# Kernel tuning notes

Measured on AMD Instinct MI355X. Metric: run time of the kernel, lower is better.

The kernel has to match this reference:

```python
import math
import jax, jax.numpy as jnp
import numpy as np

D_MODEL = 1024
N_HEADS = 16
D_FF = 4096
B = 4
T = 1024  # tgt len
S = 1024  # src len
EPS = 1e-6


def _linear_params(key, d_in, d_out):
    kw, kb = jax.random.split(key)
    w = jax.random.normal(kw, (d_out, d_in), dtype=jnp.float32) * 0.02
    b = jax.random.normal(kb, (d_out,), dtype=jnp.float32) * 0.02
    return w, b


def setup_inputs() -> dict:
    key = jax.random.key(0)
    ks = jax.random.split(key, 16)
    x = jax.random.normal(ks[0], (B, T, D_MODEL), dtype=jnp.float32)
    memory = jax.random.normal(ks[1], (B, S, D_MODEL), dtype=jnp.float32)
    # causal [B, T, T] mask (dim==3 branch) and padding [B, S] mask (dim==2 branch)
    tgt_mask = jnp.broadcast_to(jnp.tril(jnp.ones((T, T), dtype=jnp.int32)), (B, T, T))
    src_mask = jnp.ones((B, S), dtype=jnp.int32)
    inp = {"x": x, "memory": memory, "tgt_mask": tgt_mask, "src_mask": src_mask}
    names = ["sa_wq", "sa_wk", "sa_wv", "sa_wo", "ca_wq", "ca_wk", "ca_wv", "ca_wo"]
    for i, n in enumerate(names):
        w, b = _linear_params(ks[2 + i], D_MODEL, D_MODEL)
        inp[n] = w
        inp[n.replace("w", "b")] = b
    inp["ff_w1"], inp["ff_b1"] = _linear_params(ks[10], D_MODEL, D_FF)
    inp["ff_w2"], inp["ff_b2"] = _linear_params(ks[11], D_FF, D_MODEL)
    for i, n in enumerate(["ln1", "ln2", "ln3"]):
        inp[n + "_w"] = jnp.ones((D_MODEL,), dtype=jnp.float32)
        inp[n + "_b"] = jnp.zeros((D_MODEL,), dtype=jnp.float32)
    return inp


def layernorm(x, w, b):
    # torch-faithful: unbiased std (N-1), eps added to std (not variance)
    mean = jnp.mean(x, axis=-1, keepdims=True)
    d = x - mean
    std = jnp.sqrt(jnp.sum(d * d, axis=-1, keepdims=True) / (x.shape[-1] - 1))
    return w * d / (std + EPS) + b


def mha(q_in, kv_in, mask, wq, bq, wk, bk, wv, bv, wo, bo):
    Bb, Tq, D = q_in.shape
    Tk = kv_in.shape[1]
    dk = D // N_HEADS
    if mask.ndim == 2:
        mask4 = mask[:, None, None, :]
    else:
        mask4 = mask[:, None, :, :]
    q = (q_in @ wq.T + bq).reshape(Bb, Tq, N_HEADS, dk).transpose(0, 2, 1, 3)
    k = (kv_in @ wk.T + bk).reshape(Bb, Tk, N_HEADS, dk).transpose(0, 2, 1, 3)
    v = (kv_in @ wv.T + bv).reshape(Bb, Tk, N_HEADS, dk).transpose(0, 2, 1, 3)
    scores = jnp.einsum("bhqd,bhkd->bhqk", q, k) / math.sqrt(dk)
    scores = jnp.where(mask4 == 0, jnp.float32(-1e9), scores)
    attn = jax.nn.softmax(scores, axis=-1)
    out = jnp.einsum("bhqk,bhkd->bhqd", attn, v)
    out = out.transpose(0, 2, 1, 3).reshape(Bb, Tq, D)
    return out @ wo.T + bo


def reference(x, memory, tgt_mask, src_mask,
              sa_wq, sa_bq, sa_wk, sa_bk, sa_wv, sa_bv, sa_wo, sa_bo,
              ca_wq, ca_bq, ca_wk, ca_bk, ca_wv, ca_bv, ca_wo, ca_bo,
              ff_w1, ff_b1, ff_w2, ff_b2,
              ln1_w, ln1_b, ln2_w, ln2_b, ln3_w, ln3_b):
    # pre-norm decoder block (norm_first=True), dropout=0 (eval)
    h = layernorm(x, ln1_w, ln1_b)
    x = x + mha(h, h, tgt_mask, sa_wq, sa_bq, sa_wk, sa_bk, sa_wv, sa_bv, sa_wo, sa_bo)
    h = layernorm(x, ln2_w, ln2_b)
    x = x + mha(h, memory, src_mask, ca_wq, ca_bq, ca_wk, ca_bk, ca_wv, ca_bv, ca_wo, ca_bo)
    h = layernorm(x, ln3_w, ln3_b)
    x = x + (jax.nn.relu(h @ ff_w1.T + ff_b1) @ ff_w2.T + ff_b2)
    return x
```

## Files before the change

### kernel.cpp

```cpp
#include <hip/hip_runtime.h>
#include <hip/hip_bf16.h>

typedef unsigned short u16;
typedef __attribute__((ext_vector_type(4))) float f32x4;
typedef __attribute__((ext_vector_type(8))) short s16x8;
typedef __attribute__((ext_vector_type(4))) short s16x4;
typedef __attribute__((ext_vector_type(8))) __bf16 bf16x8;

#define NTOK 4096
#define DMODEL 1024
#define DFF 4096
#define NH 16
#define TSEQ 1024


__device__ __forceinline__ u16 f2b_hw(float f) {
  union { __bf16 h; u16 u; } cv;
  cv.h = (__bf16)f;
  return cv.u;
}

__device__ __forceinline__ f32x4 mfma16(s16x8 a, s16x8 b, f32x4 c) {
  return __builtin_amdgcn_mfma_f32_16x16x32_bf16((bf16x8)a, (bf16x8)b, c, 0, 0, 0);
}

__device__ __forceinline__ void gload16(const u16* g, u16* l) {
  __builtin_amdgcn_global_load_lds(
      (const __attribute__((address_space(1))) unsigned int*)g,
      (__attribute__((address_space(3))) unsigned int*)l, 16, 0, 0);
}

__device__ __forceinline__ s16x8 ld8s(const u16* t, int row, int eoff) {
  int rx = row & 7;
  const u16* p1 = t + row * 64 + ((((eoff >> 3) ^ rx) << 3) | (eoff & 7));
  const u16* p2 = t + row * 64 + (((((eoff + 16) >> 3) ^ rx) << 3) | (eoff & 7));
  s16x4 lo = *(const s16x4*)p1;
  s16x4 hi = *(const s16x4*)p2;
  s16x8 r;
  r[0] = lo[0]; r[1] = lo[1]; r[2] = lo[2]; r[3] = lo[3];
  r[4] = hi[0]; r[5] = hi[1]; r[6] = hi[2]; r[7] = hi[3];
  return r;
}

__device__ __forceinline__ s16x8 ld16s(const u16* t, int row, int ch) {
  return *(const s16x8*)(t + row * 64 + ((ch ^ (row & 7)) << 3));
}


struct F2B {
  const float* s[11];
  u16* d[11];
};

__global__ __launch_bounds__(256) void f2b_all(F2B a) {
  int bid = blockIdx.x;
  int seg, boff;
  if (bid < 8192) { seg = bid >> 10; boff = bid & 1023; }
  else { int j = bid - 8192; seg = 8 + (j >> 12); boff = j & 4095; }
  size_t i = ((size_t)boff * 256 + threadIdx.x) * 4;
  float4 v = *(const float4*)(a.s[seg] + i);
  ushort4 o = make_ushort4(f2b_hw(v.x), f2b_hw(v.y), f2b_hw(v.z), f2b_hw(v.w));
  *(ushort4*)(a.d[seg] + i) = o;
}


__global__ __launch_bounds__(256) void ln_kernel(const float* __restrict__ x,
                                                 const float* __restrict__ w,
                                                 const float* __restrict__ b,
                                                 u16* __restrict__ out) {
  int row = blockIdx.x;
  int t = threadIdx.x;
  const float* xr = x + (size_t)row * DMODEL;
  float4 v = *(const float4*)(xr + t * 4);
  float s = v.x + v.y + v.z + v.w;
#pragma unroll
  for (int off = 1; off < 64; off <<= 1) s += __shfl_xor(s, off);
  __shared__ float red[8];
  int wid = t >> 6, lane = t & 63;
  if (lane == 0) red[wid] = s;
  __syncthreads();
  float mean = (red[0] + red[1] + red[2] + red[3]) * (1.0f / 1024.0f);
  float dx = v.x - mean, dy = v.y - mean, dz = v.z - mean, dw = v.w - mean;
  float ss = dx * dx + dy * dy + dz * dz + dw * dw;
#pragma unroll
  for (int off = 1; off < 64; off <<= 1) ss += __shfl_xor(ss, off);
  if (lane == 0) red[4 + wid] = ss;
  __syncthreads();
  float sst = red[4] + red[5] + red[6] + red[7];
  float inv = 1.0f / (sqrtf(sst / 1023.0f) + 1e-6f);
  float4 wv = *(const float4*)(w + t * 4);
  float4 bv = *(const float4*)(b + t * 4);
  ushort4 o = make_ushort4(f2b_hw(wv.x * dx * inv + bv.x), f2b_hw(wv.y * dy * inv + bv.y),
                           f2b_hw(wv.z * dz * inv + bv.z), f2b_hw(wv.w * dw * inv + bv.w));
  *(ushort4*)(out + (size_t)row * DMODEL + t * 4) = o;
}


template <int MODE, bool RELU, bool SPLITK = false, int QBUF = -1, int VBUF = -1>
__global__ __launch_bounds__(512) void gemm_bt(const u16* __restrict__ A,
                                               const u16* __restrict__ W,
                                               const float* __restrict__ b0,
                                               const float* __restrict__ b1,
                                               const float* __restrict__ b2,
                                               const float* resid, void* outp,
                                               int M, int N, int K, int ld,
                                               int gx) {
  __shared__ u16 As[2][128 * 64];
  __shared__ u16 Bs[2][128 * 64];
  const int nwg = gridDim.x;
  const int qch = nwg >> 3;
  const int bid = blockIdx.x;
  int wg = (bid & 7) * qch + (bid >> 3);
  int half = 0;
  if (SPLITK) { half = wg & 1; wg >>= 1; }
  const int bx = wg % gx, by = wg / gx;
  const int m0 = by * 128, n0 = bx * 128;
  if (SPLITK) { A += (size_t)half * K; W += (size_t)half * K; }
  const int tid = threadIdx.x;
  const int wid = tid >> 6, lane = tid & 63;
  const int wr = wid >> 2, wc = wid & 3;
  const int lhi = lane >> 4, llo = lane & 15;
  f32x4 acc[4][2] = {};
  const int sr = tid >> 3, sc = tid & 7;
  const int srcoff = (sc ^ (sr & 7)) << 3;

  auto stage = [&](int kk, int buf) {
    const u16* Ap = A + (size_t)(m0 + sr) * ld + kk + srcoff;
    gload16(Ap, &As[buf][tid * 8]);
    gload16(Ap + (size_t)64 * ld, &As[buf][4096 + tid * 8]);
    const u16* Wp = W + (size_t)(n0 + sr) * ld + kk + srcoff;
    gload16(Wp, &Bs[buf][tid * 8]);
    gload16(Wp + (size_t)64 * ld, &Bs[buf][4096 + tid * 8]);
  };

  stage(0, 0);
  __syncthreads();

  for (int k0 = 0; k0 < K; k0 += 64) {
    int cur = (k0 >> 6) & 1;
    if (k0 + 64 < K) stage(k0 + 64, cur ^ 1);
#pragma unroll
    for (int ks8 = 0; ks8 < 8; ks8 += 4) {
      s16x8 af[4], bfr[2];
#pragma unroll
      for (int f = 0; f < 4; f++) af[f] = ld16s(&As[cur][0], wr * 64 + f * 16 + llo, ks8 + lhi);
#pragma unroll
      for (int g = 0; g < 2; g++) bfr[g] = ld16s(&Bs[cur][0], wc * 32 + g * 16 + llo, ks8 + lhi);
#pragma unroll
      for (int f = 0; f < 4; f++)
#pragma unroll
        for (int g = 0; g < 2; g++) acc[f][g] = mfma16(af[f], bfr[g], acc[f][g]);
    }
    __syncthreads();
  }

#pragma unroll
  for (int fm = 0; fm < 4; fm++) {
#pragma unroll
    for (int fn = 0; fn < 2; fn++) {
      int c = n0 + wc * 32 + fn * 16 + llo;
      const int r0 = m0 + wr * 64 + fm * 16 + lhi * 4;
      if (MODE == 2) {
        int buf = c >> 10, cc = c & 1023;
        int hh = cc >> 6, d = cc & 63;
        int bb = r0 >> 10, t0 = r0 & 1023;
        const float* bias = (buf == 0) ? b0 : ((buf == 1) ? b1 : b2);
        float bv = bias[cc];
        float v4[4];
#pragma unroll
        for (int i = 0; i < 4; i++) {
          float v = acc[fm][fn][i] + bv;
          if (buf == QBUF) v *= 0.125f;
          v4[i] = v;
        }
        if (buf == VBUF) {
          ushort4 st = make_ushort4(f2b_hw(v4[0]), f2b_hw(v4[1]), f2b_hw(v4[2]), f2b_hw(v4[3]));
          *(ushort4*)(&((u16*)outp)[(size_t)buf * 4194304 +
                                    (((size_t)(bb * NH + hh)) * 64 + d) * TSEQ + t0]) = st;
        } else {
#pragma unroll
          for (int i = 0; i < 4; i++)
            ((u16*)outp)[(size_t)buf * 4194304 +
                         (((size_t)(bb * NH + hh)) * TSEQ + t0 + i) * 64 + d] = f2b_hw(v4[i]);
        }
      } else {
        float bv = b0 ? b0[c] : 0.0f;
#pragma unroll
        for (int i = 0; i < 4; i++) {
          int r = r0 + i;
          float v = acc[fm][fn][i] + bv;
          if (resid) v += resid[(size_t)r * N + c];
          if (RELU) v = fmaxf(v, 0.0f);
          if (MODE == 0) {
            ((float*)outp)[(size_t)half * M * N + (size_t)r * N + c] = v;
          } else {
            ((u16*)outp)[(size_t)r * N + c] = f2b_hw(v);
          }
        }
      }
    }
  }
}


__global__ __launch_bounds__(256) void ff2_reduce(const float* __restrict__ p,
                                                  const float* __restrict__ bias,
                                                  float* __restrict__ out) {
  int row = blockIdx.x, t = threadIdx.x;
  size_t i = (size_t)row * 1024 + t * 4;
  const float* p1 = p + (size_t)4194304;
  float4 a = *(const float4*)(p + i);
  float4 b = *(const float4*)(p1 + i);
  float4 r = *(const float4*)(out + i);
  float4 bv = *(const float4*)(bias + t * 4);
  float4 o = make_float4(a.x + b.x + r.x + bv.x, a.y + b.y + r.y + bv.y,
                         a.z + b.z + r.z + bv.z, a.w + b.w + r.w + bv.w);
  *(float4*)(out + i) = o;
}


template <bool CAUSAL>
__global__ __launch_bounds__(256) void attn_kernel(const u16* __restrict__ Qg,
                                                   const u16* __restrict__ Kg,
                                                   const u16* __restrict__ Vt,
                                                   u16* __restrict__ Og) {
  const int bid = blockIdx.x;
  const int wg = (bid & 7) * 64 + (bid >> 3);
  const int bh = wg >> 3, qblk = wg & 7;
  const int b = bh >> 4, h = bh & 15;
  const int q0 = qblk * 128;
  const int tid = threadIdx.x, wid = tid >> 6, lane = tid & 63;
  const int lhi = lane >> 4, llo = lane & 15;
  __shared__ u16 Ks[2][4096];
  __shared__ u16 Vs[2][4096];

  const int qr = q0 + wid * 16 + llo;
  const u16* qp0 = Qg + ((size_t)bh * TSEQ + qr) * 64;
  s16x8 qf[2][2];
  qf[0][0] = *(const s16x8*)(qp0 + 8 * lhi);
  qf[0][1] = *(const s16x8*)(qp0 + 8 * (4 + lhi));
  qf[1][0] = *(const s16x8*)(qp0 + 4096 + 8 * lhi);
  qf[1][1] = *(const s16x8*)(qp0 + 4096 + 8 * (4 + lhi));

  f32x4 oacc[2][4] = {};
  float mrun[2] = {-1.0e30f, -1.0e30f}, lrun[2] = {0.0f, 0.0f};
  const size_t kvb = (size_t)bh * (TSEQ * 64);
  const int nt = CAUSAL ? ((q0 + 128) >> 6) : (TSEQ >> 6);

  const int srow = tid >> 3;
  const int ssw = ((tid & 7) ^ (srow & 7)) << 3;

  auto stageK = [&](int s0, int buf) {
    const u16* kb = Kg + kvb + (size_t)s0 * 64;
    gload16(kb + (size_t)srow * 64 + ssw, &Ks[buf][tid * 8]);
    gload16(kb + (size_t)(32 + srow) * 64 + ssw, &Ks[buf][2048 + tid * 8]);
  };
  auto stageV = [&](int s0, int buf) {
    const u16* vb2 = Vt + kvb + s0;
    gload16(vb2 + (size_t)srow * TSEQ + ssw, &Vs[buf][tid * 8]);
    gload16(vb2 + (size_t)(32 + srow) * TSEQ + ssw, &Vs[buf][2048 + tid * 8]);
  };

  stageK(0, 0);
  stageV(0, 0);
  __syncthreads();

  for (int t = 0; t < nt; ++t) {
    int cur = t & 1;
    if (t + 1 < nt) {
      stageK((t + 1) * 64, cur ^ 1);
      stageV((t + 1) * 64, cur ^ 1);
    }
    int s0 = t * 64;
    const bool act0 = !CAUSAL || (s0 < q0 + 64);

    s16x8 kf[4][2];
#pragma unroll
    for (int g = 0; g < 4; g++) {
      kf[g][0] = ld16s(&Ks[cur][0], g * 16 + llo, lhi);
      kf[g][1] = ld16s(&Ks[cur][0], g * 16 + llo, 4 + lhi);
    }

    s16x8 pf[2][2];
#pragma unroll
    for (int s = 0; s < 2; s++) {
      if (s == 0 && !act0) continue;
      f32x4 sacc[4] = {};
#pragma unroll
      for (int g = 0; g < 4; g++) {
        sacc[g] = mfma16(kf[g][0], qf[s][0], sacc[g]);
        sacc[g] = mfma16(kf[g][1], qf[s][1], sacc[g]);
      }
      const int qrow = qr + s * 64;
      const bool diag = CAUSAL && (s0 == q0 + s * 64);
      float sv[16];
      float pmax = -1.0e30f;
#pragma unroll
      for (int g = 0; g < 4; g++)
#pragma unroll
        for (int i = 0; i < 4; i++) {
          float sc = sacc[g][i];
          if (diag) {
            int kv = s0 + g * 16 + lhi * 4 + i;
            if (kv > qrow) sc = -1.0e9f;
          }
          sv[g * 4 + i] = sc;
          pmax = fmaxf(pmax, sc);
        }
      pmax = fmaxf(pmax, __shfl_xor(pmax, 16));
      pmax = fmaxf(pmax, __shfl_xor(pmax, 32));
      if (!__all(pmax - mrun[s] <= 8.0f)) {
        float mnew = fmaxf(mrun[s], pmax);
        float alpha = __expf(mrun[s] - mnew);
        lrun[s] *= alpha;
#pragma unroll
        for (int g = 0; g < 4; g++) {
          oacc[s][g][0] *= alpha; oacc[s][g][1] *= alpha;
          oacc[s][g][2] *= alpha; oacc[s][g][3] *= alpha;
        }
        mrun[s] = mnew;
      }
      float ls = 0.0f;
#pragma unroll
      for (int j = 0; j < 16; j++) {
        float p = __expf(sv[j] - mrun[s]);
        ls += p;
        pf[s][j >> 3][((j >> 2) & 1) * 4 + (j & 3)] = (short)f2b_hw(p);
      }
      ls += __shfl_xor(ls, 16);
      ls += __shfl_xor(ls, 32);
      lrun[s] += ls;
    }

#pragma unroll
    for (int dg = 0; dg < 4; dg++) {
      int row = dg * 16 + llo;
      s16x8 vf0 = ld8s(&Vs[cur][0], row, lhi * 4);
      s16x8 vf1 = ld8s(&Vs[cur][0], row, 32 + lhi * 4);
      if (act0) {
        oacc[0][dg] = mfma16(vf0, pf[0][0], oacc[0][dg]);
        oacc[0][dg] = mfma16(vf1, pf[0][1], oacc[0][dg]);
      }
      oacc[1][dg] = mfma16(vf0, pf[1][0], oacc[1][dg]);
      oacc[1][dg] = mfma16(vf1, pf[1][1], oacc[1][dg]);
    }

    __syncthreads();
  }

#pragma unroll
  for (int s = 0; s < 2; s++) {
    float inv = 1.0f / lrun[s];
    u16* orow = Og + (size_t)(b * TSEQ + qr + s * 64) * DMODEL + h * 64;
#pragma unroll
    for (int dg = 0; dg < 4; dg++) {
      ushort4 st = make_ushort4(f2b_hw(oacc[s][dg][0] * inv), f2b_hw(oacc[s][dg][1] * inv),
                                f2b_hw(oacc[s][dg][2] * inv), f2b_hw(oacc[s][dg][3] * inv));
      *(ushort4*)(orow + dg * 16 + lhi * 4) = st;
    }
  }
}


extern "C" void kernel_launch(void* const* d_in, const int* in_sizes, int n_in,
                              void* d_out, int out_size, void* d_ws, size_t ws_size,
                              hipStream_t stream) {
  const float* x      = (const float*)d_in[0];
  const float* memory = (const float*)d_in[1];
  const float* sa_wq = (const float*)d_in[4];  const float* sa_bq = (const float*)d_in[5];
  const float* sa_wk = (const float*)d_in[6];  const float* sa_bk = (const float*)d_in[7];
  const float* sa_wv = (const float*)d_in[8];  const float* sa_bv = (const float*)d_in[9];
  const float* sa_wo = (const float*)d_in[10]; const float* sa_bo = (const float*)d_in[11];
  const float* ca_wq = (const float*)d_in[12]; const float* ca_bq = (const float*)d_in[13];
  const float* ca_wk = (const float*)d_in[14]; const float* ca_bk = (const float*)d_in[15];
  const float* ca_wv = (const float*)d_in[16]; const float* ca_bv = (const float*)d_in[17];
  const float* ca_wo = (const float*)d_in[18]; const float* ca_bo = (const float*)d_in[19];
  const float* ff_w1 = (const float*)d_in[20]; const float* ff_b1 = (const float*)d_in[21];
  const float* ff_w2 = (const float*)d_in[22]; const float* ff_b2 = (const float*)d_in[23];
  const float* ln1_w = (const float*)d_in[24]; const float* ln1_b = (const float*)d_in[25];
  const float* ln2_w = (const float*)d_in[26]; const float* ln2_b = (const float*)d_in[27];
  const float* ln3_w = (const float*)d_in[28]; const float* ln3_b = (const float*)d_in[29];
  float* out = (float*)d_out;

  char* ws = (char*)d_ws;
  const size_t MB = 1u << 20;
  u16* h_bf   = (u16*)(ws + 0 * MB);
  u16* mem_bf = (u16*)(ws + 8 * MB);
  u16* qb     = (u16*)(ws + 16 * MB);
  u16* kb     = (u16*)(ws + 24 * MB);
  u16* vb     = (u16*)(ws + 32 * MB);
  u16* attnb  = (u16*)(ws + 40 * MB);
  u16* ffmid  = (u16*)(ws + 48 * MB);
  float* pk   = (float*)(ws + 16 * MB);
  u16* w_sq   = (u16*)(ws + 80 * MB);
  u16* w_sk   = (u16*)(ws + 82 * MB);
  u16* w_sv   = (u16*)(ws + 84 * MB);
  u16* w_so   = (u16*)(ws + 86 * MB);
  u16* w_cq   = (u16*)(ws + 88 * MB);
  u16* w_ck   = (u16*)(ws + 90 * MB);
  u16* w_cv   = (u16*)(ws + 92 * MB);
  u16* w_co   = (u16*)(ws + 94 * MB);
  u16* w_f1   = (u16*)(ws + 96 * MB);
  u16* w_f2   = (u16*)(ws + 104 * MB);

  F2B fa;
  fa.s[0] = sa_wq; fa.d[0] = w_sq;
  fa.s[1] = sa_wk; fa.d[1] = w_sk;
  fa.s[2] = sa_wv; fa.d[2] = w_sv;
  fa.s[3] = sa_wo; fa.d[3] = w_so;
  fa.s[4] = ca_wq; fa.d[4] = w_cq;
  fa.s[5] = ca_wk; fa.d[5] = w_ck;
  fa.s[6] = ca_wv; fa.d[6] = w_cv;
  fa.s[7] = ca_wo; fa.d[7] = w_co;
  fa.s[8] = ff_w1; fa.d[8] = w_f1;
  fa.s[9] = ff_w2; fa.d[9] = w_f2;
  fa.s[10] = memory; fa.d[10] = mem_bf;
  f2b_all<<<20480, 256, 0, stream>>>(fa);

  ln_kernel<<<4096, 256, 0, stream>>>(x, ln1_w, ln1_b, h_bf);
  gemm_bt<2, false, false, 0, 2><<<768, 512, 0, stream>>>(
      h_bf, w_sq, sa_bq, sa_bk, sa_bv, nullptr, qb, NTOK, 3072, DMODEL, DMODEL, 24);
  attn_kernel<true><<<512, 256, 0, stream>>>(qb, kb, vb, attnb);
  gemm_bt<0, false><<<256, 512, 0, stream>>>(attnb, w_so, sa_bo, nullptr, nullptr,
                                             x, out, NTOK, DMODEL, DMODEL, DMODEL, 8);

  ln_kernel<<<4096, 256, 0, stream>>>(out, ln2_w, ln2_b, h_bf);
  gemm_bt<2, false, false, 0, -1><<<256, 512, 0, stream>>>(
      h_bf, w_cq, ca_bq, nullptr, nullptr, nullptr, qb, NTOK, DMODEL, DMODEL, DMODEL, 8);
  gemm_bt<2, false, false, -1, 1><<<512, 512, 0, stream>>>(
      mem_bf, w_ck, ca_bk, ca_bv, nullptr, nullptr, kb, NTOK, 2048, DMODEL, DMODEL, 16);
  attn_kernel<false><<<512, 256, 0, stream>>>(qb, kb, vb, attnb);
  gemm_bt<0, false><<<256, 512, 0, stream>>>(attnb, w_co, ca_bo, nullptr, nullptr,
                                             out, out, NTOK, DMODEL, DMODEL, DMODEL, 8);

  ln_kernel<<<4096, 256, 0, stream>>>(out, ln3_w, ln3_b, h_bf);
  gemm_bt<1, true><<<1024, 512, 0, stream>>>(h_bf, w_f1, ff_b1, nullptr, nullptr,
                                             nullptr, ffmid, NTOK, DFF, DMODEL, DMODEL, 32);
  gemm_bt<0, false, true><<<512, 512, 0, stream>>>(ffmid, w_f2, nullptr, nullptr, nullptr,
                                                   nullptr, pk, NTOK, DMODEL, 2048, DFF, 8);
  ff2_reduce<<<4096, 256, 0, stream>>>(pk, ff_b2, out);

  (void)in_sizes; (void)n_in; (void)out_size; (void)ws_size;
}
```

Baseline: 332.8 us.

## Add 128x256-tile triple-buffered GEMM kernel for wide projection GEMMs

```diff
diff --git a/kernel.cpp b/kernel.cpp
--- a/kernel.cpp
+++ b/kernel.cpp
@@ -12,6 +12,8 @@
 #define DFF 4096
 #define NH 16
 #define TSEQ 1024
+
+#define SBAR() do { asm volatile("" ::: "memory"); __builtin_amdgcn_s_barrier(); asm volatile("" ::: "memory"); } while (0)
 
 
 __device__ __forceinline__ u16 f2b_hw(float f) {
@@ -93,6 +95,127 @@
   ushort4 o = make_ushort4(f2b_hw(wv.x * dx * inv + bv.x), f2b_hw(wv.y * dy * inv + bv.y),
                            f2b_hw(wv.z * dz * inv + bv.z), f2b_hw(wv.w * dw * inv + bv.w));
   *(ushort4*)(out + (size_t)row * DMODEL + t * 4) = o;
+}
+
+
+template <int MODE, bool RELU, int QBUF, int VBUF>
+__global__ __launch_bounds__(512, 2) void gemm_big(const u16* __restrict__ A,
+                                                   const u16* __restrict__ W,
+                                                   const float* __restrict__ b0,
+                                                   const float* __restrict__ b1,
+                                                   const float* __restrict__ b2,
+                                                   void* outp,
+                                                   int M, int N, int K, int ld,
+                                                   int gx) {
+  __shared__ u16 As[3][128 * 64];
+  __shared__ u16 Bs[3][256 * 64];
+  const int nwg = gridDim.x, qch = nwg >> 3, bid = blockIdx.x;
+  const int wg = (bid & 7) * qch + (bid >> 3);
+  const int bx = wg % gx, by = wg / gx;
+  const int m0 = by * 128, n0 = bx * 256;
+  const int tid = threadIdx.x;
+  const int wid = tid >> 6, lane = tid & 63;
+  const int wr = wid >> 2, wc = wid & 3;
+  const int lhi = lane >> 4, llo = lane & 15;
+  f32x4 acc[4][4] = {};
+
+  auto stageA = [&](int t, int buf, int j) {
+    int s = j * 512 + tid;
+    int row = s >> 3, c = s & 7;
+    gload16(A + (size_t)(m0 + row) * ld + t * 64 + ((c ^ (row & 7)) << 3),
+            &As[buf][s * 8]);
+  };
+  auto stageB = [&](int t, int buf, int j) {
+    int s = j * 512 + tid;
+    int row = s >> 3, c = s & 7;
+    gload16(W + (size_t)(n0 + row) * ld + t * 64 + ((c ^ (row & 7)) << 3),
+            &Bs[buf][s * 8]);
+  };
+
+  const int NT = K >> 6;
+  stageA(0, 0, 0); stageA(0, 0, 1);
+  stageB(0, 0, 0); stageB(0, 0, 1); stageB(0, 0, 2); stageB(0, 0, 3);
+  stageA(1, 1, 0); stageA(1, 1, 1);
+  stageB(1, 1, 0); stageB(1, 1, 1); stageB(1, 1, 2); stageB(1, 1, 3);
+  asm volatile("s_waitcnt vmcnt(6)" ::: "memory");
+  SBAR();
+
+  int cur = 0;
+#pragma unroll 1
+  for (int t = 0; t < NT; ++t) {
+    const int nb = (cur >= 1) ? cur - 1 : 2;
+    const bool pf2 = (t + 2 < NT);
+#pragma unroll
+    for (int kk = 0; kk < 2; ++kk) {
+      s16x8 af[4], bf[4];
+#pragma unroll
+      for (int fm = 0; fm < 4; fm++)
+        af[fm] = ld16s(&As[cur][0], wr * 64 + fm * 16 + llo, kk * 4 + lhi);
+#pragma unroll
+      for (int fn = 0; fn < 4; fn++)
+        bf[fn] = ld16s(&Bs[cur][0], wc * 64 + fn * 16 + llo, kk * 4 + lhi);
+      if (pf2) {
+        if (kk == 0) { stageA(t + 2, nb, 0); stageA(t + 2, nb, 1); stageB(t + 2, nb, 0); }
+        else         { stageB(t + 2, nb, 1); stageB(t + 2, nb, 2); stageB(t + 2, nb, 3); }
+      }
+      SBAR();
+      __builtin_amdgcn_s_setprio(1);
+#pragma unroll
+      for (int fm = 0; fm < 4; fm++)
+#pragma unroll
+        for (int fn = 0; fn < 4; fn++)
+          acc[fm][fn] = mfma16(af[fm], bf[fn], acc[fm][fn]);
+      __builtin_amdgcn_s_setprio(0);
+      if (kk == 1) {
+        if (pf2) asm volatile("s_waitcnt vmcnt(6)" ::: "memory");
+        else if (t + 1 < NT) asm volatile("s_waitcnt vmcnt(0)" ::: "memory");
+      }
+      SBAR();
+    }
+    cur = (cur == 2) ? 0 : cur + 1;
+  }
+
+#pragma unroll
+  for (int fm = 0; fm < 4; fm++) {
+#pragma unroll
+    for (int fn = 0; fn < 4; fn++) {
+      int c = n0 + wc * 64 + fn * 16 + llo;
+      int r0 = m0 + wr * 64 + fm * 16 + lhi * 4;
+      if (MODE == 2) {
+        int buf = c >> 10, cc = c & 1023;
+        int hh = cc >> 6, d = cc & 63;
+        int bb = r0 >> 10, t0 = r0 & 1023;
+        const float* bias = (buf == 0) ? b0 : ((buf == 1) ? b1 : b2);
+        float bv = bias[cc];
+        float v4[4];
+#pragma unroll
+        for (int i = 0; i < 4; i++) {
+          float v = acc[fm][fn][i] + bv;
+          if (buf == QBUF) v *= 0.125f;
+          v4[i] = v;
+        }
+        if (buf == VBUF) {
+          ushort4 st = make_ushort4(f2b_hw(v4[0]), f2b_hw(v4[1]), f2b_hw(v4[2]), f2b_hw(v4[3]));
+          *(ushort4*)(&((u16*)outp)[(size_t)buf * 4194304 +
+                                    (((size_t)(bb * NH + hh)) * 64 + d) * TSEQ + t0]) = st;
+        } else {
+#pragma unroll
+          for (int i = 0; i < 4; i++)
+            ((u16*)outp)[(size_t)buf * 4194304 +
+                         (((size_t)(bb * NH + hh)) * TSEQ + t0 + i) * 64 + d] = f2b_hw(v4[i]);
+        }
+      } else {
+        float bv = b0[c];
+#pragma unroll
+        for (int i = 0; i < 4; i++) {
+          float v = acc[fm][fn][i] + bv;
+          if (RELU) v = fmaxf(v, 0.0f);
+          ((u16*)outp)[(size_t)(r0 + i) * N + c] = f2b_hw(v);
+        }
+      }
+    }
+  }
+  (void)M;
 }
 
 
@@ -418,8 +541,8 @@
   f2b_all<<<20480, 256, 0, stream>>>(fa);
 
   ln_kernel<<<4096, 256, 0, stream>>>(x, ln1_w, ln1_b, h_bf);
-  gemm_bt<2, false, false, 0, 2><<<768, 512, 0, stream>>>(
-      h_bf, w_sq, sa_bq, sa_bk, sa_bv, nullptr, qb, NTOK, 3072, DMODEL, DMODEL, 24);
+  gemm_big<2, false, 0, 2><<<384, 512, 0, stream>>>(
+      h_bf, w_sq, sa_bq, sa_bk, sa_bv, qb, NTOK, 3072, DMODEL, DMODEL, 12);
   attn_kernel<true><<<512, 256, 0, stream>>>(qb, kb, vb, attnb);
   gemm_bt<0, false><<<256, 512, 0, stream>>>(attnb, w_so, sa_bo, nullptr, nullptr,
                                              x, out, NTOK, DMODEL, DMODEL, DMODEL, 8);
@@ -427,15 +550,15 @@
   ln_kernel<<<4096, 256, 0, stream>>>(out, ln2_w, ln2_b, h_bf);
   gemm_bt<2, false, false, 0, -1><<<256, 512, 0, stream>>>(
       h_bf, w_cq, ca_bq, nullptr, nullptr, nullptr, qb, NTOK, DMODEL, DMODEL, DMODEL, 8);
-  gemm_bt<2, false, false, -1, 1><<<512, 512, 0, stream>>>(
-      mem_bf, w_ck, ca_bk, ca_bv, nullptr, nullptr, kb, NTOK, 2048, DMODEL, DMODEL, 16);
+  gemm_big<2, false, -1, 1><<<256, 512, 0, stream>>>(
+      mem_bf, w_ck, ca_bk, ca_bv, ca_bv, kb, NTOK, 2048, DMODEL, DMODEL, 8);
   attn_kernel<false><<<512, 256, 0, stream>>>(qb, kb, vb, attnb);
   gemm_bt<0, false><<<256, 512, 0, stream>>>(attnb, w_co, ca_bo, nullptr, nullptr,
                                              out, out, NTOK, DMODEL, DMODEL, DMODEL, 8);
 
   ln_kernel<<<4096, 256, 0, stream>>>(out, ln3_w, ln3_b, h_bf);
-  gemm_bt<1, true><<<1024, 512, 0, stream>>>(h_bf, w_f1, ff_b1, nullptr, nullptr,
-                                             nullptr, ffmid, NTOK, DFF, DMODEL, DMODEL, 32);
+  gemm_big<1, true, -1, -1><<<512, 512, 0, stream>>>(
+      h_bf, w_f1, ff_b1, nullptr, nullptr, ffmid, NTOK, DFF, DMODEL, DMODEL, 16);
   gemm_bt<0, false, true><<<512, 512, 0, stream>>>(ffmid, w_f2, nullptr, nullptr, nullptr,
                                                    nullptr, pk, NTOK, DMODEL, 2048, DFF, 8);
   ff2_reduce<<<4096, 256, 0, stream>>>(pk, ff_b2, out);
```

After: 340.2 us. 2.2% more time.

## Add 256-thread 128x128 GEMM with K=32 stages for projection and FFN GEMMs

Applied to the files above, without the earlier changes.

```diff
diff --git a/kernel.cpp b/kernel.cpp
--- a/kernel.cpp
+++ b/kernel.cpp
@@ -46,6 +46,10 @@
   return *(const s16x8*)(t + row * 64 + ((ch ^ (row & 7)) << 3));
 }
 
+__device__ __forceinline__ s16x8 ld16s32(const u16* t, int row, int ch) {
+  return *(const s16x8*)(t + row * 32 + ((ch ^ ((row >> 1) & 3)) << 3));
+}
+
 
 struct F2B {
   const float* s[11];
@@ -97,19 +101,17 @@
 
 
 template <int MODE, bool RELU, bool SPLITK = false, int QBUF = -1, int VBUF = -1>
-__global__ __launch_bounds__(512) void gemm_bt(const u16* __restrict__ A,
+__global__ __launch_bounds__(256) void gemm128(const u16* __restrict__ A,
                                                const u16* __restrict__ W,
                                                const float* __restrict__ b0,
                                                const float* __restrict__ b1,
                                                const float* __restrict__ b2,
-                                               const float* resid, void* outp,
+                                               void* outp,
                                                int M, int N, int K, int ld,
                                                int gx) {
-  __shared__ u16 As[2][128 * 64];
-  __shared__ u16 Bs[2][128 * 64];
-  const int nwg = gridDim.x;
-  const int qch = nwg >> 3;
-  const int bid = blockIdx.x;
+  __shared__ u16 As[2][128 * 32];
+  __shared__ u16 Bs[2][128 * 32];
+  const int nwg = gridDim.x, qch = nwg >> 3, bid = blockIdx.x;
   int wg = (bid & 7) * qch + (bid >> 3);
   int half = 0;
   if (SPLITK) { half = wg & 1; wg >>= 1; }
@@ -118,47 +120,44 @@
   if (SPLITK) { A += (size_t)half * K; W += (size_t)half * K; }
   const int tid = threadIdx.x;
   const int wid = tid >> 6, lane = tid & 63;
-  const int wr = wid >> 2, wc = wid & 3;
+  const int wr = wid >> 1, wc = wid & 1;
   const int lhi = lane >> 4, llo = lane & 15;
-  f32x4 acc[4][2] = {};
-  const int sr = tid >> 3, sc = tid & 7;
-  const int srcoff = (sc ^ (sr & 7)) << 3;
+  f32x4 acc[4][4] = {};
+  const int sr = tid >> 2, sc = tid & 3;
+  const int srcoff = (sc ^ ((sr >> 1) & 3)) << 3;
 
   auto stage = [&](int kk, int buf) {
     const u16* Ap = A + (size_t)(m0 + sr) * ld + kk + srcoff;
     gload16(Ap, &As[buf][tid * 8]);
-    gload16(Ap + (size_t)64 * ld, &As[buf][4096 + tid * 8]);
+    gload16(Ap + (size_t)64 * ld, &As[buf][2048 + tid * 8]);
     const u16* Wp = W + (size_t)(n0 + sr) * ld + kk + srcoff;
     gload16(Wp, &Bs[buf][tid * 8]);
-    gload16(Wp + (size_t)64 * ld, &Bs[buf][4096 + tid * 8]);
+    gload16(Wp + (size_t)64 * ld, &Bs[buf][2048 + tid * 8]);
   };
 
   stage(0, 0);
   __syncthreads();
 
-  for (int k0 = 0; k0 < K; k0 += 64) {
-    int cur = (k0 >> 6) & 1;
-    if (k0 + 64 < K) stage(k0 + 64, cur ^ 1);
-#pragma unroll
-    for (int ks8 = 0; ks8 < 8; ks8 += 4) {
-      s16x8 af[4], bfr[2];
-#pragma unroll
-      for (int f = 0; f < 4; f++) af[f] = ld16s(&As[cur][0], wr * 64 + f * 16 + llo, ks8 + lhi);
-#pragma unroll
-      for (int g = 0; g < 2; g++) bfr[g] = ld16s(&Bs[cur][0], wc * 32 + g * 16 + llo, ks8 + lhi);
-#pragma unroll
-      for (int f = 0; f < 4; f++)
-#pragma unroll
-        for (int g = 0; g < 2; g++) acc[f][g] = mfma16(af[f], bfr[g], acc[f][g]);
-    }
+  for (int k0 = 0; k0 < K; k0 += 32) {
+    int cur = (k0 >> 5) & 1;
+    if (k0 + 32 < K) stage(k0 + 32, cur ^ 1);
+    s16x8 af[4], bf[4];
+#pragma unroll
+    for (int f = 0; f < 4; f++) af[f] = ld16s32(&As[cur][0], wr * 64 + f * 16 + llo, lhi);
+#pragma unroll
+    for (int g = 0; g < 4; g++) bf[g] = ld16s32(&Bs[cur][0], wc * 64 + g * 16 + llo, lhi);
+#pragma unroll
+    for (int f = 0; f < 4; f++)
+#pragma unroll
+      for (int g = 0; g < 4; g++) acc[f][g] = mfma16(af[f], bf[g], acc[f][g]);
     __syncthreads();
   }
 
 #pragma unroll
   for (int fm = 0; fm < 4; fm++) {
 #pragma unroll
-    for (int fn = 0; fn < 2; fn++) {
-      int c = n0 + wc * 32 + fn * 16 + llo;
+    for (int fn = 0; fn < 4; fn++) {
+      int c = n0 + wc * 64 + fn * 16 + llo;
       const int r0 = m0 + wr * 64 + fm * 16 + lhi * 4;
       if (MODE == 2) {
         int buf = c >> 10, cc = c & 1023;
@@ -187,15 +186,90 @@
         float bv = b0 ? b0[c] : 0.0f;
 #pragma unroll
         for (int i = 0; i < 4; i++) {
-          int r = r0 + i;
           float v = acc[fm][fn][i] + bv;
-          if (resid) v += resid[(size_t)r * N + c];
           if (RELU) v = fmaxf(v, 0.0f);
           if (MODE == 0) {
-            ((float*)outp)[(size_t)half * M * N + (size_t)r * N + c] = v;
+            ((float*)outp)[(size_t)half * M * N + (size_t)(r0 + i) * N + c] = v;
           } else {
-            ((u16*)outp)[(size_t)r * N + c] = f2b_hw(v);
+            ((u16*)outp)[(size_t)(r0 + i) * N + c] = f2b_hw(v);
           }
+        }
+      }
+    }
+  }
+}
+
+
+template <int MODE, bool RELU>
+__global__ __launch_bounds__(512) void gemm_bt(const u16* __restrict__ A,
+                                               const u16* __restrict__ W,
+                                               const float* __restrict__ b0,
+                                               const float* resid, void* outp,
+                                               int M, int N, int K, int ld,
+                                               int gx) {
+  __shared__ u16 As[2][128 * 64];
+  __shared__ u16 Bs[2][128 * 64];
+  const int nwg = gridDim.x;
+  const int qch = nwg >> 3;
+  const int bid = blockIdx.x;
+  int wg = (bid & 7) * qch + (bid >> 3);
+  const int bx = wg % gx, by = wg / gx;
+  const int m0 = by * 128, n0 = bx * 128;
+  const int tid = threadIdx.x;
+  const int wid = tid >> 6, lane = tid & 63;
+  const int wr = wid >> 2, wc = wid & 3;
+  const int lhi = lane >> 4, llo = lane & 15;
+  f32x4 acc[4][2] = {};
+  const int sr = tid >> 3, sc = tid & 7;
+  const int srcoff = (sc ^ (sr & 7)) << 3;
+
+  auto stage = [&](int kk, int buf) {
+    const u16* Ap = A + (size_t)(m0 + sr) * ld + kk + srcoff;
+    gload16(Ap, &As[buf][tid * 8]);
+    gload16(Ap + (size_t)64 * ld, &As[buf][4096 + tid * 8]);
+    const u16* Wp = W + (size_t)(n0 + sr) * ld + kk + srcoff;
+    gload16(Wp, &Bs[buf][tid * 8]);
+    gload16(Wp + (size_t)64 * ld, &Bs[buf][4096 + tid * 8]);
+  };
+
+  stage(0, 0);
+  __syncthreads();
+
+  for (int k0 = 0; k0 < K; k0 += 64) {
+    int cur = (k0 >> 6) & 1;
+    if (k0 + 64 < K) stage(k0 + 64, cur ^ 1);
+#pragma unroll
+    for (int ks8 = 0; ks8 < 8; ks8 += 4) {
+      s16x8 af[4], bfr[2];
+#pragma unroll
+      for (int f = 0; f < 4; f++) af[f] = ld16s(&As[cur][0], wr * 64 + f * 16 + llo, ks8 + lhi);
+#pragma unroll
+      for (int g = 0; g < 2; g++) bfr[g] = ld16s(&Bs[cur][0], wc * 32 + g * 16 + llo, ks8 + lhi);
+#pragma unroll
+      for (int f = 0; f < 4; f++)
+#pragma unroll
+        for (int g = 0; g < 2; g++) acc[f][g] = mfma16(af[f], bfr[g], acc[f][g]);
+    }
+    __syncthreads();
+  }
+
+#pragma unroll
+  for (int fm = 0; fm < 4; fm++) {
+#pragma unroll
+    for (int fn = 0; fn < 2; fn++) {
+      int c = n0 + wc * 32 + fn * 16 + llo;
+      const int r0 = m0 + wr * 64 + fm * 16 + lhi * 4;
+      float bv = b0 ? b0[c] : 0.0f;
+#pragma unroll
+      for (int i = 0; i < 4; i++) {
+        int r = r0 + i;
+        float v = acc[fm][fn][i] + bv;
+        if (resid) v += resid[(size_t)r * N + c];
+        if (RELU) v = fmaxf(v, 0.0f);
+        if (MODE == 0) {
+          ((float*)outp)[(size_t)r * N + c] = v;
+        } else {
+          ((u16*)outp)[(size_t)r * N + c] = f2b_hw(v);
         }
       }
     }
@@ -418,26 +492,26 @@
   f2b_all<<<20480, 256, 0, stream>>>(fa);
 
   ln_kernel<<<4096, 256, 0, stream>>>(x, ln1_w, ln1_b, h_bf);
-  gemm_bt<2, false, false, 0, 2><<<768, 512, 0, stream>>>(
-      h_bf, w_sq, sa_bq, sa_bk, sa_bv, nullptr, qb, NTOK, 3072, DMODEL, DMODEL, 24);
+  gemm128<2, false, false, 0, 2><<<768, 256, 0, stream>>>(
+      h_bf, w_sq, sa_bq, sa_bk, sa_bv, qb, NTOK, 3072, DMODEL, DMODEL, 24);
   attn_kernel<true><<<512, 256, 0, stream>>>(qb, kb, vb, attnb);
-  gemm_bt<0, false><<<256, 512, 0, stream>>>(attnb, w_so, sa_bo, nullptr, nullptr,
+  gemm_bt<0, false><<<256, 512, 0, stream>>>(attnb, w_so, sa_bo,
                                              x, out, NTOK, DMODEL, DMODEL, DMODEL, 8);
 
   ln_kernel<<<4096, 256, 0, stream>>>(out, ln2_w, ln2_b, h_bf);
-  gemm_bt<2, false, false, 0, -1><<<256, 512, 0, stream>>>(
-      h_bf, w_cq, ca_bq, nullptr, nullptr, nullptr, qb, NTOK, DMODEL, DMODEL, DMODEL, 8);
-  gemm_bt<2, false, false, -1, 1><<<512, 512, 0, stream>>>(
-      mem_bf, w_ck, ca_bk, ca_bv, nullptr, nullptr, kb, NTOK, 2048, DMODEL, DMODEL, 16);
+  gemm128<2, false, false, 0, -1><<<256, 256, 0, stream>>>(
+      h_bf, w_cq, ca_bq, nullptr, nullptr, qb, NTOK, DMODEL, DMODEL, DMODEL, 8);
+  gemm128<2, false, false, -1, 1><<<512, 256, 0, stream>>>(
+      mem_bf, w_ck, ca_bk, ca_bv, nullptr, kb, NTOK, 2048, DMODEL, DMODEL, 16);
   attn_kernel<false><<<512, 256, 0, stream>>>(qb, kb, vb, attnb);
-  gemm_bt<0, false><<<256, 512, 0, stream>>>(attnb, w_co, ca_bo, nullptr, nullptr,
+  gemm_bt<0, false><<<256, 512, 0, stream>>>(attnb, w_co, ca_bo,
                                              out, out, NTOK, DMODEL, DMODEL, DMODEL, 8);
 
   ln_kernel<<<4096, 256, 0, stream>>>(out, ln3_w, ln3_b, h_bf);
-  gemm_bt<1, true><<<1024, 512, 0, stream>>>(h_bf, w_f1, ff_b1, nullptr, nullptr,
-                                             nullptr, ffmid, NTOK, DFF, DMODEL, DMODEL, 32);
-  gemm_bt<0, false, true><<<512, 512, 0, stream>>>(ffmid, w_f2, nullptr, nullptr, nullptr,
-                                                   nullptr, pk, NTOK, DMODEL, 2048, DFF, 8);
+  gemm128<1, true><<<1024, 256, 0, stream>>>(
+      h_bf, w_f1, ff_b1, nullptr, nullptr, ffmid, NTOK, DFF, DMODEL, DMODEL, 32);
+  gemm128<0, false, true><<<512, 256, 0, stream>>>(
+      ffmid, w_f2, nullptr, nullptr, nullptr, pk, NTOK, DMODEL, 2048, DFF, 8);
   ff2_reduce<<<4096, 256, 0, stream>>>(pk, ff_b2, out);
 
   (void)in_sizes; (void)n_in; (void)out_size; (void)ws_size;
```

After: 363.5 us. 9.2% more time.
